# Performance work log

Measured on AMD Instinct MI355X. Metric: run time of the kernel, lower is better.

## Reference

```python
import jax, jax.numpy as jnp
import numpy as np
from jax import lax

NL = 32            # number of ocean layers
NFORCING = 720     # hourly forcing steps (30 days)
DT_FORCING = 3600.0
DT = 60.0
NSUB = 60          # dt_forcing // dt
FC_VAL = 1e-4      # Coriolis frequency [s^-1]


def setup_inputs() -> dict:
    key = jax.random.key(0)
    k1, k2, k3 = jax.random.split(key, 3)
    # pk = log(K); keep K in a physically sane range via offset
    pk = jax.random.normal(k1, (2 * NL,), dtype=jnp.float32) * 0.5 - 10.0
    TAx = jax.random.normal(k2, (NFORCING,), dtype=jnp.float32) * 0.1  # wind stress [N/m^2]
    TAy = jax.random.normal(k3, (NFORCING,), dtype=jnp.float32) * 0.1
    fc = jnp.full((1,), FC_VAL, dtype=jnp.float32)
    return {"pk": pk, "TAx": TAx, "TAy": TAy, "fc": fc}


def _vector_field(t, U, V, f, K, TAx, TAy):
    # temporal interpolation of forcing (matches original index arithmetic)
    it = jnp.asarray(t // DT, jnp.int32)
    itf = it // NSUB
    aa = (jnp.mod(it, NSUB) / NSUB).astype(U.dtype)
    nT = TAx.shape[0]
    itsup = jnp.where(itf + 1 >= nT, -1, itf + 1)
    TAxnow = (1 - aa) * TAx[itf] + aa * TAx[itsup]
    TAynow = (1 - aa) * TAy[itf] + aa * TAy[itsup]
    # N-layer stencil (nl > 1 branch of lax.cond), fully vectorized:
    #   layer 0   : +Kin[0]*TA       - Kout[0]*(x0 - x1)
    #   layer k   : -Kin[k]*(xk-xk-1) - Kout[k]*(xk - xk+1)
    #   layer nl-1: -Kin[-1]*(x - x_prev) - Kout[-1]*x   (i.e. x_next = 0)
    Kin, Kout = K[0::2], K[1::2]                       # [nl] each
    zero = jnp.zeros((1,), U.dtype)
    Unext = jnp.concatenate([U[1:], zero])
    Vnext = jnp.concatenate([V[1:], zero])
    dU_top = jnp.concatenate([Kin[:1] * TAxnow, -Kin[1:] * (U[1:] - U[:-1])])
    dV_top = jnp.concatenate([Kin[:1] * TAynow, -Kin[1:] * (V[1:] - V[:-1])])
    d_U = f * V + dU_top - Kout * (U - Unext)
    d_V = -f * U + dV_top - Kout * (V - Vnext)
    return d_U, d_V


def reference(pk, TAx, TAy, fc):
    nl = pk.shape[0] // 2
    K = jnp.exp(pk)
    f = fc[0]
    Nforcing = TAx.shape[0]
    U0 = jnp.zeros((Nforcing, nl), dtype=pk.dtype)
    V0 = jnp.zeros((Nforcing, nl), dtype=pk.dtype)

    def inner(carry, iin):
        Uold, Vold, iout = carry
        t = iout * DT_FORCING + iin * DT
        d_U, d_V = _vector_field(t, Uold, Vold, f, K, TAx, TAy)
        return (Uold + DT * d_U, Vold + DT * d_V, iout), None

    def outer(carry, iout):
        U, V = carry
        (u, v, _), _ = lax.scan(inner, (U[iout], V[iout], iout),
                                jnp.arange(NSUB))
        # last write (iout+1 == Nforcing) is out-of-bounds -> dropped,
        # exactly as in the original .at[].set semantics
        U = U.at[iout + 1].set(u)
        V = V.at[iout + 1].set(v)
        return (U, V), None

    (U, V), _ = lax.scan(outer, (U0, V0), jnp.arange(Nforcing))
    return U, V
```

## Files before the change

kernel.cpp:

```cpp
#include <hip/hip_runtime.h>
#include <hip/hip_bf16.h>

#define NLAYERS 32
#define NFORC   720
#define NSUB    60
#define DTS     60.0f
#define T_CH    16
#define N_CH    45
#define MAGIC   0x1234ABCD
#define SD      34


__device__ __forceinline__ bool sniff_bf16(const void* pk_raw, int lane) {
    const __hip_bfloat16* pk_bf = (const __hip_bfloat16*)pk_raw;
    const float v = __bfloat162float(pk_bf[lane]);
    return __all(v > -30.0f && v < -1.0f);
}

__device__ __forceinline__ void load_mrow(const float2* sMat, int i, int h, float2* R) {
    const float4* rp = (const float4*)(sMat + i * SD + h * 16);
    #pragma unroll
    for (int jj = 0; jj < 8; ++jj) {
        const float4 v = rp[jj];
        R[2 * jj]     = make_float2(v.x, v.y);
        R[2 * jj + 1] = make_float2(v.z, v.w);
    }
}

__device__ __forceinline__ float2 rmatvec(const float2* R, float2 x, int hbase) {
    float a0 = 0.f, a1 = 0.f, a2 = 0.f, a3 = 0.f;
    #pragma unroll
    for (int jj = 0; jj < 16; ++jj) {
        const float xr = __shfl(x.x, hbase + jj);
        const float xi = __shfl(x.y, hbase + jj);
        const float2 m = R[jj];
        a0 = fmaf(m.x, xr, a0);
        a1 = fmaf(m.y, xi, a1);
        a2 = fmaf(m.x, xi, a2);
        a3 = fmaf(m.y, xr, a3);
    }
    float yr = a0 - a1, yi = a2 + a3;
    yr += __shfl_xor(yr, 32);
    yi += __shfl_xor(yi, 32);
    return make_float2(yr, yi);
}

__device__ __forceinline__ void cmatmul8(float2* D, const float2* A, const float2* B, int tt) {
    if ((unsigned)tt < 128u) {
        const int i = tt >> 2, j0 = (tt & 3) * 8;
        float ar[8], ai[8];
        #pragma unroll
        for (int m = 0; m < 8; ++m) { ar[m] = 0.f; ai[m] = 0.f; }
        #pragma unroll 4
        for (int k = 0; k < 32; ++k) {
            const float2 a = A[i * SD + k];
            const float4* bp = (const float4*)(B + k * SD + j0);
            #pragma unroll
            for (int m = 0; m < 4; ++m) {
                const float4 b = bp[m];
                ar[2*m]   = fmaf(a.x, b.x, fmaf(-a.y, b.y, ar[2*m]));
                ai[2*m]   = fmaf(a.x, b.y, fmaf( a.y, b.x, ai[2*m]));
                ar[2*m+1] = fmaf(a.x, b.z, fmaf(-a.y, b.w, ar[2*m+1]));
                ai[2*m+1] = fmaf(a.x, b.w, fmaf( a.y, b.z, ai[2*m+1]));
            }
        }
        float4* dp = (float4*)(D + i * SD + j0);
        #pragma unroll
        for (int m = 0; m < 4; ++m)
            dp[m] = make_float4(ar[2*m], ai[2*m], ar[2*m+1], ai[2*m+1]);
    }
}

__global__ __launch_bounds__(1024, 1)
void junsteak_one(const void* pk_raw, const void* tax_raw, const void* tay_raw,
                  const void* fc_raw, float2* ws_z, int* ws_flag, void* out_raw)
{
    __shared__ __align__(16) float2 sM [NLAYERS * SD];
    __shared__ __align__(16) float2 sB1[NLAYERS * SD];
    __shared__ __align__(16) float2 sB2[NLAYERS * SD];
    __shared__ __align__(16) float2 sCX[NFORC];
    __shared__ __align__(16) float2 sZL[(N_CH - 1) * NLAYERS];
    __shared__ __align__(16) float4 sPQ[NLAYERS];

    const int t = threadIdx.x, lane = t & 63, wv = t >> 6;
    const int l = lane & 31, h = lane >> 5, col = 2 * wv + h;
    const int c = blockIdx.x;
    const int hbase = 16 * h;

    const bool bf = sniff_bf16(pk_raw, lane);

    float kin, kout, f, dtkin0;
    if (bf) {
        const __hip_bfloat16* pk = (const __hip_bfloat16*)pk_raw;
        kin    = expf(__bfloat162float(pk[2 * l]));
        kout   = expf(__bfloat162float(pk[2 * l + 1]));
        f      = __bfloat162float(((const __hip_bfloat16*)fc_raw)[0]);
        dtkin0 = DTS * expf(__bfloat162float(pk[0]));
        const __hip_bfloat16* tx = (const __hip_bfloat16*)tax_raw;
        const __hip_bfloat16* ty = (const __hip_bfloat16*)tay_raw;
        if (t < NFORC)
            sCX[t] = make_float2(__bfloat162float(tx[t]), __bfloat162float(ty[t]));
    } else {
        const float* pk = (const float*)pk_raw;
        kin    = expf(pk[2 * l]);
        kout   = expf(pk[2 * l + 1]);
        f      = ((const float*)fc_raw)[0];
        dtkin0 = DTS * expf(pk[0]);
        const float* tx = (const float*)tax_raw;
        const float* ty = (const float*)tay_raw;
        if (t < NFORC) sCX[t] = make_float2(tx[t], ty[t]);
    }

    __hip_bfloat16* out_bf = (__hip_bfloat16*)out_raw;
    float*          out_f  = (float*)out_raw;
    const int VOFF = NFORC * NLAYERS;

    if (c == 0 && t < 64) {
        const int off = (t >= 32 ? VOFF : 0) + (t & 31);
        if (bf) out_bf[off] = __float2bfloat16(0.0f); else out_f[off] = 0.0f;
    }

    {
        float xr = (l == col) ? 1.0f : 0.0f, xi = 0.0f;
        float Pr = 0.f, Pi = 0.f, Qr = 0.f, Qi = 0.f;
        const bool row0 = (l == 0), row31 = (l == 31);
        for (int m = 0; m < NSUB; ++m) {
            const float cp = dtkin0 * (float)(m + 1) * (1.0f / 60.0f);
            const float cq = dtkin0 * (float)(NSUB - 1 - m) * (1.0f / 60.0f);
            Pr = fmaf(cp, xr, Pr); Pi = fmaf(cp, xi, Pi);
            Qr = fmaf(cq, xr, Qr); Qi = fmaf(cq, xi, Qi);
            float xrm = __shfl_up(xr, 1);
            float xim = __shfl_up(xi, 1);
            float xrp = __shfl_down(xr, 1);
            float xip = __shfl_down(xi, 1);
            if (row31) { xrp = 0.0f; xip = 0.0f; }
            const float Lr = row0 ? (-kout * (xr - xrp))
                                  : (-kin * (xr - xrm) - kout * (xr - xrp));
            const float Li = row0 ? (-kout * (xi - xip))
                                  : (-kin * (xi - xim) - kout * (xi - xip));
            const float nxr = xr + DTS * Lr + DTS * f * xi;
            const float nxi = xi + DTS * Li - DTS * f * xr;
            xr = nxr; xi = nxi;
        }
        sM[l * SD + col] = make_float2(xr, xi);
        if (wv == 0 && h == 0) sPQ[l] = make_float4(Pr, Pi, Qr, Qi);
    }
    __syncthreads();

    float4 pq = make_float4(0.f, 0.f, 0.f, 0.f);
    float2 Mreg[16];
    float2 x = make_float2(0.0f, 0.0f);
    const int a    = c * T_CH;
    const int bend = min(a + T_CH, NFORC - 1);

    if (wv == 0) {
        pq = sPQ[l];
        load_mrow(sM, l, h, Mreg);
        float2 cn = sCX[a];
        for (int s = a; s < bend; ++s) {
            const float2 cs = cn;
            cn = sCX[s + 1];
            const float2 y = rmatvec(Mreg, x, hbase);
            const float gr = pq.x * cs.x - pq.y * cs.y + pq.z * cn.x - pq.w * cn.y;
            const float gi = pq.x * cs.y + pq.y * cs.x + pq.z * cn.y + pq.w * cn.x;
            x = make_float2(y.x + gr, y.y + gi);
        }
        if (h == 0) {
            unsigned long long zu;
            __builtin_memcpy(&zu, &x, 8);
            __hip_atomic_store((unsigned long long*)(ws_z + c * NLAYERS + l), zu,
                               __ATOMIC_RELAXED, __HIP_MEMORY_SCOPE_AGENT);
        }
        __threadfence();
        if (lane == 0)
            __hip_atomic_store(ws_flag + c, (int)MAGIC,
                               __ATOMIC_RELEASE, __HIP_MEMORY_SCOPE_AGENT);
    } else {
        cmatmul8(sB1, sM, sM, t - 64);
    }
    __syncthreads();

    if (wv == 0) {
        if (c > 0) {
            int v;
            do {
                v = (lane < c) ? __hip_atomic_load(ws_flag + lane, __ATOMIC_ACQUIRE,
                                                   __HIP_MEMORY_SCOPE_AGENT)
                               : (int)MAGIC;
            } while (!__all(v == (int)MAGIC));
            for (int idx = lane; idx < c * NLAYERS; idx += 64) {
                const unsigned long long zu =
                    __hip_atomic_load((const unsigned long long*)(ws_z + idx),
                                      __ATOMIC_RELAXED, __HIP_MEMORY_SCOPE_AGENT);
                float2 z;
                __builtin_memcpy(&z, &zu, 8);
                sZL[idx] = z;
            }
        }
    } else {
        cmatmul8(sB2, sB1, sB1, t - 64);
    }
    __syncthreads();

    if (wv != 0) cmatmul8(sB1, sB2, sB2, t - 64);
    __syncthreads();
    if (wv != 0) cmatmul8(sB2, sB1, sB1, t - 64);
    __syncthreads();

    if (t >= 64) return;

    {
        float2 Ereg[16];
        load_mrow(sB2, l, h, Ereg);
        x = make_float2(0.0f, 0.0f);
        for (int j = 0; j < c; ++j) {
            const float2 z = sZL[j * NLAYERS + l];
            const float2 y = rmatvec(Ereg, x, hbase);
            x = make_float2(y.x + z.x, y.y + z.y);
        }
    }

    {
        float2 cn = sCX[a];
        for (int s = a; s < bend; ++s) {
            const float2 cs = cn;
            cn = sCX[s + 1];
            const float2 y = rmatvec(Mreg, x, hbase);
            const float gr = pq.x * cs.x - pq.y * cs.y + pq.z * cn.x - pq.w * cn.y;
            const float gi = pq.x * cs.y + pq.y * cs.x + pq.z * cn.y + pq.w * cn.x;
            x = make_float2(y.x + gr, y.y + gi);
            if (h == 0) {
                const int row = (s + 1) * NLAYERS + l;
                if (bf) {
                    out_bf[row]        = __float2bfloat16(x.x);
                    out_bf[VOFF + row] = __float2bfloat16(x.y);
                } else {
                    out_f[row]        = x.x;
                    out_f[VOFF + row] = x.y;
                }
            }
        }
    }
}

extern "C" void kernel_launch(void* const* d_in, const int* in_sizes, int n_in,
                              void* d_out, int out_size, void* d_ws, size_t ws_size,
                              hipStream_t stream) {
    (void)in_sizes; (void)n_in; (void)out_size; (void)ws_size;
    float2* ws_z   = (float2*)d_ws;
    int*    ws_flg = (int*)((char*)d_ws + (size_t)N_CH * NLAYERS * sizeof(float2));
    junsteak_one<<<dim3(N_CH), dim3(1024), 0, stream>>>(
        d_in[0], d_in[1], d_in[2], d_in[3], ws_z, ws_flg, d_out);
}
```

Measured before the change: 112.7 us.

## Parallelize chunk fix-up across waves using stored particular solutions and matrix powers

Instead of wave 0 serially re-running each chunk's recurrence after receiving the carry-in, the kernel stores the zero-initial particular solution per step and applies the carry-in via precomputed matrix powers (M, M^2, M^4, M^8, M^16), so each wave computes one or two output steps in parallel. Block-wide __syncthreads are replaced with LDS flag counters and spin-waits with s_sleep so that squaring, the inter-block wait and the carry-in solve can overlap. Chunk size grows to 24 steps and the number of blocks drops to 30, which shortens the serial carry-in chain. The trade-offs are more LDS usage, more matrix squarings, and spin-wait overheads.

```diff
diff --git a/kernel.cpp b/kernel.cpp
--- a/kernel.cpp
+++ b/kernel.cpp
@@ -5,8 +5,8 @@
 #define NFORC   720
 #define NSUB    60
 #define DTS     60.0f
-#define T_CH    16
-#define N_CH    45
+#define T_CH    24
+#define N_CH    30
 #define MAGIC   0x1234ABCD
 #define SD      34
 
@@ -45,47 +45,65 @@
     return make_float2(yr, yi);
 }
 
+__device__ __forceinline__ float2 rmatvec_lds(const float2* mat, float2 x,
+                                              int l, int h, int hbase) {
+    float2 R[16];
+    load_mrow(mat, l, h, R);
+    return rmatvec(R, x, hbase);
+}
+
 __device__ __forceinline__ void cmatmul8(float2* D, const float2* A, const float2* B, int tt) {
-    if ((unsigned)tt < 128u) {
-        const int i = tt >> 2, j0 = (tt & 3) * 8;
-        float ar[8], ai[8];
+    const int i = tt >> 2, j0 = (tt & 3) * 8;
+    float ar[8], ai[8];
+    #pragma unroll
+    for (int m = 0; m < 8; ++m) { ar[m] = 0.f; ai[m] = 0.f; }
+    #pragma unroll 4
+    for (int k = 0; k < 32; ++k) {
+        const float2 a = A[i * SD + k];
+        const float4* bp = (const float4*)(B + k * SD + j0);
         #pragma unroll
-        for (int m = 0; m < 8; ++m) { ar[m] = 0.f; ai[m] = 0.f; }
-        #pragma unroll 4
-        for (int k = 0; k < 32; ++k) {
-            const float2 a = A[i * SD + k];
-            const float4* bp = (const float4*)(B + k * SD + j0);
-            #pragma unroll
-            for (int m = 0; m < 4; ++m) {
-                const float4 b = bp[m];
-                ar[2*m]   = fmaf(a.x, b.x, fmaf(-a.y, b.y, ar[2*m]));
-                ai[2*m]   = fmaf(a.x, b.y, fmaf( a.y, b.x, ai[2*m]));
-                ar[2*m+1] = fmaf(a.x, b.z, fmaf(-a.y, b.w, ar[2*m+1]));
-                ai[2*m+1] = fmaf(a.x, b.w, fmaf( a.y, b.z, ai[2*m+1]));
-            }
-        }
-        float4* dp = (float4*)(D + i * SD + j0);
-        #pragma unroll
-        for (int m = 0; m < 4; ++m)
-            dp[m] = make_float4(ar[2*m], ai[2*m], ar[2*m+1], ai[2*m+1]);
-    }
+        for (int m = 0; m < 4; ++m) {
+            const float4 b = bp[m];
+            ar[2*m]   = fmaf(a.x, b.x, fmaf(-a.y, b.y, ar[2*m]));
+            ai[2*m]   = fmaf(a.x, b.y, fmaf( a.y, b.x, ai[2*m]));
+            ar[2*m+1] = fmaf(a.x, b.z, fmaf(-a.y, b.w, ar[2*m+1]));
+            ai[2*m+1] = fmaf(a.x, b.w, fmaf( a.y, b.z, ai[2*m+1]));
+        }
+    }
+    float4* dp = (float4*)(D + i * SD + j0);
+    #pragma unroll
+    for (int m = 0; m < 4; ++m)
+        dp[m] = make_float4(ar[2*m], ai[2*m], ar[2*m+1], ai[2*m+1]);
+}
+
+__device__ __forceinline__ void lds_wait_ge(int* p, int target) {
+    while (__hip_atomic_load(p, __ATOMIC_ACQUIRE, __HIP_MEMORY_SCOPE_WORKGROUP) < target)
+        __builtin_amdgcn_s_sleep(8);
 }
 
 __global__ __launch_bounds__(1024, 1)
 void junsteak_one(const void* pk_raw, const void* tax_raw, const void* tay_raw,
                   const void* fc_raw, float2* ws_z, int* ws_flag, void* out_raw)
 {
-    __shared__ __align__(16) float2 sM [NLAYERS * SD];
-    __shared__ __align__(16) float2 sB1[NLAYERS * SD];
-    __shared__ __align__(16) float2 sB2[NLAYERS * SD];
-    __shared__ __align__(16) float2 sCX[NFORC];
-    __shared__ __align__(16) float2 sZL[(N_CH - 1) * NLAYERS];
-    __shared__ __align__(16) float4 sPQ[NLAYERS];
+    __shared__ __align__(16) float2 sM  [NLAYERS * SD];
+    __shared__ __align__(16) float2 sL2 [NLAYERS * SD];
+    __shared__ __align__(16) float2 sL4 [NLAYERS * SD];
+    __shared__ __align__(16) float2 sL8 [NLAYERS * SD];
+    __shared__ __align__(16) float2 sL16[NLAYERS * SD];
+    __shared__ __align__(16) float2 sE  [NLAYERS * SD];
+    __shared__ __align__(16) float2 sCX [NFORC];
+    __shared__ __align__(16) float2 sP1 [T_CH * NLAYERS];
+    __shared__ __align__(16) float2 sZL [(N_CH - 1) * NLAYERS];
+    __shared__ __align__(16) float2 sBC [NLAYERS];
+    __shared__ __align__(16) float4 sPQ [NLAYERS];
+    __shared__ int sLad, sZrdy, sBrdy;
 
     const int t = threadIdx.x, lane = t & 63, wv = t >> 6;
     const int l = lane & 31, h = lane >> 5, col = 2 * wv + h;
     const int c = blockIdx.x;
     const int hbase = 16 * h;
+
+    if (t == 0) { sLad = 0; sZrdy = 0; sBrdy = 0; }
 
     const bool bf = sniff_bf16(pk_raw, lane);
 
@@ -147,14 +165,14 @@
     }
     __syncthreads();
 
-    float4 pq = make_float4(0.f, 0.f, 0.f, 0.f);
-    float2 Mreg[16];
+    const int a      = c * T_CH;
+    const int bend   = min(a + T_CH, NFORC - 1);
+    const int nsteps = bend - a;
     float2 x = make_float2(0.0f, 0.0f);
-    const int a    = c * T_CH;
-    const int bend = min(a + T_CH, NFORC - 1);
 
     if (wv == 0) {
-        pq = sPQ[l];
+        const float4 pq = sPQ[l];
+        float2 Mreg[16];
         load_mrow(sM, l, h, Mreg);
         float2 cn = sCX[a];
         for (int s = a; s < bend; ++s) {
@@ -164,6 +182,7 @@
             const float gr = pq.x * cs.x - pq.y * cs.y + pq.z * cn.x - pq.w * cn.y;
             const float gi = pq.x * cs.y + pq.y * cs.x + pq.z * cn.y + pq.w * cn.x;
             x = make_float2(y.x + gr, y.y + gi);
+            if (h == 0) sP1[(s - a) * NLAYERS + l] = x;
         }
         if (h == 0) {
             unsigned long long zu;
@@ -175,19 +194,47 @@
         if (lane == 0)
             __hip_atomic_store(ws_flag + c, (int)MAGIC,
                                __ATOMIC_RELEASE, __HIP_MEMORY_SCOPE_AGENT);
-    } else {
-        cmatmul8(sB1, sM, sM, t - 64);
-    }
-    __syncthreads();
-
-    if (wv == 0) {
+
+        lds_wait_ge(&sLad, 10);
+        lds_wait_ge(&sZrdy, 1);
+
+        float2 Ereg[16];
+        load_mrow(sE, l, h, Ereg);
+        x = make_float2(0.0f, 0.0f);
+        for (int j = 0; j < c; ++j) {
+            const float2 z = sZL[j * NLAYERS + l];
+            const float2 y = rmatvec(Ereg, x, hbase);
+            x = make_float2(y.x + z.x, y.y + z.y);
+        }
+        if (h == 0) sBC[l] = x;
+        if (lane == 0)
+            __hip_atomic_store(&sBrdy, 1, __ATOMIC_RELEASE, __HIP_MEMORY_SCOPE_WORKGROUP);
+    } else if (wv == 1 || wv == 2) {
+        const int tt = t - 64;
+        cmatmul8(sL2,  sM,  sM,  tt);
+        if (lane == 0) __hip_atomic_fetch_add(&sLad, 1, __ATOMIC_ACQ_REL, __HIP_MEMORY_SCOPE_WORKGROUP);
+        lds_wait_ge(&sLad, 2);
+        cmatmul8(sL4,  sL2, sL2, tt);
+        if (lane == 0) __hip_atomic_fetch_add(&sLad, 1, __ATOMIC_ACQ_REL, __HIP_MEMORY_SCOPE_WORKGROUP);
+        lds_wait_ge(&sLad, 4);
+        cmatmul8(sL8,  sL4, sL4, tt);
+        if (lane == 0) __hip_atomic_fetch_add(&sLad, 1, __ATOMIC_ACQ_REL, __HIP_MEMORY_SCOPE_WORKGROUP);
+        lds_wait_ge(&sLad, 6);
+        cmatmul8(sL16, sL8, sL8, tt);
+        if (lane == 0) __hip_atomic_fetch_add(&sLad, 1, __ATOMIC_ACQ_REL, __HIP_MEMORY_SCOPE_WORKGROUP);
+        lds_wait_ge(&sLad, 8);
+        cmatmul8(sE,   sL16, sL8, tt);
+        if (lane == 0) __hip_atomic_fetch_add(&sLad, 1, __ATOMIC_ACQ_REL, __HIP_MEMORY_SCOPE_WORKGROUP);
+    } else if (wv == 3) {
         if (c > 0) {
             int v;
             do {
                 v = (lane < c) ? __hip_atomic_load(ws_flag + lane, __ATOMIC_ACQUIRE,
                                                    __HIP_MEMORY_SCOPE_AGENT)
                                : (int)MAGIC;
-            } while (!__all(v == (int)MAGIC));
+                if (!__all(v == (int)MAGIC)) __builtin_amdgcn_s_sleep(8);
+                else break;
+            } while (true);
             for (int idx = lane; idx < c * NLAYERS; idx += 64) {
                 const unsigned long long zu =
                     __hip_atomic_load((const unsigned long long*)(ws_z + idx),
@@ -197,48 +244,39 @@
                 sZL[idx] = z;
             }
         }
-    } else {
-        cmatmul8(sB2, sB1, sB1, t - 64);
-    }
-    __syncthreads();
-
-    if (wv != 0) cmatmul8(sB1, sB2, sB2, t - 64);
-    __syncthreads();
-    if (wv != 0) cmatmul8(sB2, sB1, sB1, t - 64);
-    __syncthreads();
-
-    if (t >= 64) return;
-
+        if (lane == 0)
+            __hip_atomic_store(&sZrdy, 1, __ATOMIC_RELEASE, __HIP_MEMORY_SCOPE_WORKGROUP);
+    }
+
+    if (wv != 0) lds_wait_ge(&sBrdy, 1);
+
+    const float2 b = (wv == 0) ? x : sBC[l];
+
+    float2 corr = b;
     {
-        float2 Ereg[16];
-        load_mrow(sB2, l, h, Ereg);
-        x = make_float2(0.0f, 0.0f);
-        for (int j = 0; j < c; ++j) {
-            const float2 z = sZL[j * NLAYERS + l];
-            const float2 y = rmatvec(Ereg, x, hbase);
-            x = make_float2(y.x + z.x, y.y + z.y);
-        }
-    }
-
-    {
-        float2 cn = sCX[a];
-        for (int s = a; s < bend; ++s) {
-            const float2 cs = cn;
-            cn = sCX[s + 1];
-            const float2 y = rmatvec(Mreg, x, hbase);
-            const float gr = pq.x * cs.x - pq.y * cs.y + pq.z * cn.x - pq.w * cn.y;
-            const float gi = pq.x * cs.y + pq.y * cs.x + pq.z * cn.y + pq.w * cn.x;
-            x = make_float2(y.x + gr, y.y + gi);
-            if (h == 0) {
-                const int row = (s + 1) * NLAYERS + l;
-                if (bf) {
-                    out_bf[row]        = __float2bfloat16(x.x);
-                    out_bf[VOFF + row] = __float2bfloat16(x.y);
-                } else {
-                    out_f[row]        = x.x;
-                    out_f[VOFF + row] = x.y;
-                }
-            }
+        const int e = wv + 1;
+        if (e & 1)  corr = rmatvec_lds(sM,   corr, l, h, hbase);
+        if (e & 2)  corr = rmatvec_lds(sL2,  corr, l, h, hbase);
+        if (e & 4)  corr = rmatvec_lds(sL4,  corr, l, h, hbase);
+        if (e & 8)  corr = rmatvec_lds(sL8,  corr, l, h, hbase);
+        if (e & 16) corr = rmatvec_lds(sL16, corr, l, h, hbase);
+    }
+    if (wv < nsteps && h == 0) {
+        const float2 st = sP1[wv * NLAYERS + l];
+        const int row = (a + wv + 1) * NLAYERS + l;
+        const float u = st.x + corr.x, vv = st.y + corr.y;
+        if (bf) { out_bf[row] = __float2bfloat16(u); out_bf[VOFF + row] = __float2bfloat16(vv); }
+        else    { out_f[row] = u;                    out_f[VOFF + row] = vv; }
+    }
+    const int m2 = wv + 16;
+    if (m2 < T_CH) {
+        corr = rmatvec_lds(sL16, corr, l, h, hbase);
+        if (m2 < nsteps && h == 0) {
+            const float2 st = sP1[m2 * NLAYERS + l];
+            const int row = (a + m2 + 1) * NLAYERS + l;
+            const float u = st.x + corr.x, vv = st.y + corr.y;
+            if (bf) { out_bf[row] = __float2bfloat16(u); out_bf[VOFF + row] = __float2bfloat16(vv); }
+            else    { out_f[row] = u;                    out_f[VOFF + row] = vv; }
         }
     }
 }
```

Measured after the change: 101.5 us. 1.11x faster.
